# Optimization experiments

Measured on AMD Instinct MI355X. Metric: run time of the kernel, lower is better.

Reference implementation:

```python
import jax, jax.numpy as jnp
import numpy as np

N_NODES = 20000
N_EDGES = 160000
IN_DIM = 2048
HID = 512


def setup_inputs() -> dict:
    key = jax.random.key(0)
    ks = jax.random.split(key, 12)
    s1 = 1.0 / np.sqrt(IN_DIM)
    s2 = 1.0 / np.sqrt(HID)
    return {
        "x": jax.random.normal(ks[0], (N_NODES, IN_DIM), dtype=jnp.float32),
        "edge_index": jax.random.randint(ks[1], (2, N_EDGES), 0, N_NODES, dtype=jnp.int64),
        "W1": jax.random.uniform(ks[2], (IN_DIM, HID), jnp.float32, -s1, s1),
        "b1": jax.random.uniform(ks[3], (HID,), jnp.float32, -s1, s1),
        "W2": jax.random.uniform(ks[4], (HID, HID), jnp.float32, -s2, s2),
        "b2": jax.random.uniform(ks[5], (HID,), jnp.float32, -s2, s2),
        "Wg": jax.random.uniform(ks[6], (HID, HID), jnp.float32, -s2, s2),
        "bg": jax.random.uniform(ks[7], (HID,), jnp.float32, -s2, s2),
        "Wa": jax.random.uniform(ks[8], (HID, 1), jnp.float32, -s2, s2),
        "ba": jax.random.uniform(ks[9], (1,), jnp.float32, -s2, s2),
    }


def reference(x, edge_index, W1, b1, W2, b2, Wg, bg, Wa, ba):
    # GINConv (eps=0): h = MLP((1+eps)*x + sum_{j in N(i)} x_j)
    src, dst = edge_index[0], edge_index[1]
    agg = jax.ops.segment_sum(x[src], dst, num_segments=x.shape[0])  # [N, IN_DIM]
    h = x + agg
    h = jnp.maximum(h @ W1 + b1, 0.0) @ W2 + b2  # [N, HID]
    # Gated attention pooling scores
    A = jnp.tanh(h @ Wg + bg)                    # [N, HID]
    alpha = (A @ Wa + ba)[:, 0]                  # [N]
    att_scores = jax.nn.softmax(alpha, axis=0)   # softmax over all nodes
    return (h, att_scores)
```

## Files before the change

kernel.cpp:

```cpp
#include <hip/hip_runtime.h>

typedef __attribute__((ext_vector_type(8))) __bf16 bf16x8;
typedef __attribute__((ext_vector_type(4))) __bf16 bf16x4;
typedef __attribute__((ext_vector_type(4))) float f32x4;
typedef __attribute__((ext_vector_type(8))) unsigned short u16x8;

__device__ __forceinline__ bf16x8 cvt8(float4 a, float4 b) {
    bf16x8 o;
    o[0] = (__bf16)a.x; o[1] = (__bf16)a.y; o[2] = (__bf16)a.z; o[3] = (__bf16)a.w;
    o[4] = (__bf16)b.x; o[5] = (__bf16)b.y; o[6] = (__bf16)b.z; o[7] = (__bf16)b.w;
    return o;
}
__device__ __forceinline__ bf16x4 cvt4(f32x4 v) {
    bf16x4 o;
    o[0] = (__bf16)v[0]; o[1] = (__bf16)v[1]; o[2] = (__bf16)v[2]; o[3] = (__bf16)v[3];
    return o;
}

__device__ __forceinline__ unsigned swz(int row, int s) {
    return (unsigned)((row * 64 + s * 16) ^ ((row & 8) << 2));
}

__global__ __launch_bounds__(256) void convw_pre_kernel(const float* __restrict__ W,
                                                        char* __restrict__ out, int K) {
    int t = blockIdx.x * 256 + threadIdx.x;
    if (t >= K * 512) return;
    int k = t >> 9, n = t & 511;
    int cb = n >> 8, r = n & 255, tt = k >> 5, s = (k & 31) >> 3, e = k & 7;
    size_t off = ((size_t)cb * (K >> 5) + tt) * 16384 + swz(r, s) + e * 2;
    *(__bf16*)(out + off) = (__bf16)W[t];
}

__global__ __launch_bounds__(256) void count_kernel(const int* __restrict__ dst,
                                                    int* __restrict__ counts, int E) {
    int e = blockIdx.x * 256 + threadIdx.x;
    if (e < E) atomicAdd(&counts[dst[e]], 1);
}

__global__ __launch_bounds__(1024) void scan_kernel(const int* __restrict__ counts,
                                                    int* __restrict__ offs, int N) {
    __shared__ int wsum[16], wpre[16];
    const int CH = 20;
    int tid = threadIdx.x, lane = tid & 63, wv = tid >> 6;
    int base = tid * CH;
    int s = 0;
    for (int i = 0; i < CH; i++) { int idx = base + i; s += (idx < N) ? counts[idx] : 0; }
    int run = s;
#pragma unroll
    for (int o = 1; o < 64; o <<= 1) { int v = __shfl_up(run, o, 64); if (lane >= o) run += v; }
    if (lane == 63) wsum[wv] = run;
    __syncthreads();
    if (tid == 0) { int acc = 0; for (int w = 0; w < 16; w++) { wpre[w] = acc; acc += wsum[w]; } }
    __syncthreads();
    int pre = wpre[wv] + (run - s);
    for (int i = 0; i < CH; i++) {
        int idx = base + i;
        if (idx <= N) offs[idx] = pre;
        pre += (idx < N) ? counts[idx] : 0;
    }
}

__global__ __launch_bounds__(256) void bucket_kernel(const int* __restrict__ src,
                                                     const int* __restrict__ dst,
                                                     const int* __restrict__ offs,
                                                     int* __restrict__ cursor,
                                                     int* __restrict__ eids, int E) {
    int e = blockIdx.x * 256 + threadIdx.x;
    if (e >= E) return;
    int d = dst[e];
    int pos = atomicAdd(&cursor[d], 1);
    eids[offs[d] + pos] = src[e];
}

__global__ __launch_bounds__(256) void gather_h1_kernel(const float* __restrict__ y,
                                                        const int* __restrict__ offs,
                                                        const int* __restrict__ eids,
                                                        const float* __restrict__ b1,
                                                        __bf16* __restrict__ h1b,
                                                        int N) {
    int node = blockIdx.x * 2 + (threadIdx.x >> 7);
    if (node >= N) return;
    int c = (threadIdx.x & 127) << 2;
    float4 s = *(const float4*)(y + (size_t)node * 512 + c);
    int beg = offs[node], end = offs[node + 1];
    for (int k = beg; k < end; k++) {
        int sn = eids[k];
        const float4 v = *(const float4*)(y + (size_t)sn * 512 + c);
        s.x += v.x; s.y += v.y; s.z += v.z; s.w += v.w;
    }
    const float4 b = *(const float4*)(b1 + c);
    f32x4 r;
    r[0] = fmaxf(s.x + b.x, 0.f);
    r[1] = fmaxf(s.y + b.y, 0.f);
    r[2] = fmaxf(s.z + b.z, 0.f);
    r[3] = fmaxf(s.w + b.w, 0.f);
    *(bf16x4*)(h1b + (size_t)node * 512 + c) = cvt4(r);
}

__global__ __launch_bounds__(256) void gemm1_kernel(const float* __restrict__ X,
                                                    const char* __restrict__ Bpre,
                                                    float* __restrict__ Y, int M) {
    constexpr int KDIM = 2048, NT2 = KDIM / 64;
    __shared__ char smem[16384];
    const int tid = threadIdx.x, lane = tid & 63, wv = tid >> 6;
    const int fr = lane & 15, sec = lane >> 4, hi4 = (lane >> 4) * 4;
    const long row0 = (long)blockIdx.x * 64;
    const char* Bp = Bpre + (size_t)blockIdx.y * 64 * 16384;

    f32x4 acc[4][4];
#pragma unroll
    for (int m = 0; m < 4; m++)
#pragma unroll
        for (int n = 0; n < 4; n++)
#pragma unroll
            for (int r = 0; r < 4; r++) acc[m][n][r] = 0.f;

    const int ar_ = tid >> 2, ks = tid & 3;
    const unsigned awz = swz(ar_, ks);
    long arow = row0 + ar_; if (arow > (long)M - 1) arow = M - 1;
    const float* Ap = X + arow * KDIM;

#define ASEC(b) (smem + (b) * 8192)
#define LOAD_A(d0, d1, d2, d3, t) do {                       \
        const float* p_ = Ap + (t) * 64 + ks * 8;            \
        d0 = *(const float4*)(p_);                           \
        d1 = *(const float4*)(p_ + 4);                       \
        d2 = *(const float4*)(p_ + 32);                      \
        d3 = *(const float4*)(p_ + 36);                      \
    } while (0)
#define LOAD_WF(dst, g) do {                                              \
        const char* bt_ = Bp + (size_t)(g) * 16384;                       \
        _Pragma("unroll") for (int m_ = 0; m_ < 4; m_++)                  \
            dst[m_] = *(const bf16x8*)(bt_ + swz(wv * 64 + m_ * 16 + fr, sec)); \
    } while (0)

    float4 aP0, aP1, aP2, aP3, aN0, aN1, aN2, aN3;
    bf16x8 wfC[4], wfN[4];

    LOAD_A(aP0, aP1, aP2, aP3, 0);
    *(bf16x8*)(ASEC(0) + awz) = cvt8(aP0, aP1);
    *(bf16x8*)(ASEC(0) + 4096 + awz) = cvt8(aP2, aP3);
    LOAD_A(aP0, aP1, aP2, aP3, 1);
    LOAD_A(aN0, aN1, aN2, aN3, 2);
    LOAD_WF(wfC, 0);
    asm volatile("s_waitcnt lgkmcnt(0)" ::: "memory");
    __builtin_amdgcn_s_barrier();

    int cur = 0;
    for (int tt = 0; tt < NT2; tt++) {
#pragma unroll
        for (int h = 0; h < 2; h++) {
            const int g = tt * 2 + h;
            if (g + 1 < NT2 * 2) LOAD_WF(wfN, g + 1);
            bf16x8 xf[4];
#pragma unroll
            for (int n = 0; n < 4; n++)
                xf[n] = *(const bf16x8*)(ASEC(cur) + h * 4096 + swz(n * 16 + fr, sec));
#pragma unroll
            for (int m = 0; m < 4; m++)
#pragma unroll
                for (int n = 0; n < 4; n++)
                    acc[m][n] = __builtin_amdgcn_mfma_f32_16x16x32_bf16(wfC[m], xf[n], acc[m][n], 0, 0, 0);
#pragma unroll
            for (int m = 0; m < 4; m++) wfC[m] = wfN[m];
        }
        if (tt + 1 < NT2) {
            const int nxt = cur ^ 1;
            *(bf16x8*)(ASEC(nxt) + awz) = cvt8(aP0, aP1);
            *(bf16x8*)(ASEC(nxt) + 4096 + awz) = cvt8(aP2, aP3);
            aP0 = aN0; aP1 = aN1; aP2 = aN2; aP3 = aN3;
            if (tt + 3 < NT2) LOAD_A(aN0, aN1, aN2, aN3, tt + 3);
            asm volatile("s_waitcnt lgkmcnt(0)" ::: "memory");
            __builtin_amdgcn_s_barrier();
            cur = nxt;
        }
    }
#undef ASEC
#undef LOAD_A
#undef LOAD_WF

#pragma unroll
    for (int n = 0; n < 4; n++) {
        long node = row0 + n * 16 + fr;
        if (node < M) {
#pragma unroll
            for (int m = 0; m < 4; m++)
                *(f32x4*)(Y + node * 512 + blockIdx.y * 256 + wv * 64 + m * 16 + hi4) = acc[m][n];
        }
    }
}

__global__ __launch_bounds__(512) void mlp23_kernel(const __bf16* __restrict__ H1,
                                                    const char* __restrict__ W2p,
                                                    const float* __restrict__ b2,
                                                    const char* __restrict__ Wgp,
                                                    const float* __restrict__ bg,
                                                    const float* __restrict__ Wa,
                                                    float* __restrict__ Hout,
                                                    float* __restrict__ alpha) {
    constexpr int NT2 = 8;
    __shared__ char smem[41216];
    char* Hs = smem + 8192;
    float* aS = (float*)(smem + 40960);
    const int tid = threadIdx.x, lane = tid & 63, wv = tid >> 6;
    const int fr = lane & 15, sec = lane >> 4, hi4 = (lane >> 4) * 4;
    const long row0 = (long)blockIdx.x * 32;
    const int cbv = wv >> 2, rbase = (wv & 3) * 64;

    if (tid < 32) aS[tid] = 0.f;

    const int srow = tid >> 3, sh = (tid & 7) >> 2, ss = tid & 3;
    const unsigned awz = (unsigned)(sh * 2048) + swz(srow, ss);
    const __bf16* ApH = H1 + (row0 + srow) * 512 + sh * 32 + ss * 8;

#define ASEC(b) (smem + (b) * 4096)
#define LOAD_WF(dst, img, g) do {                                         \
        const char* bt_ = (img) + ((size_t)cbv * 16 + (g)) * 16384;       \
        _Pragma("unroll") for (int m_ = 0; m_ < 4; m_++)                  \
            dst[m_] = *(const bf16x8*)(bt_ + swz(rbase + m_ * 16 + fr, sec)); \
    } while (0)

    f32x4 acc[4][2];
#pragma unroll
    for (int m = 0; m < 4; m++)
#pragma unroll
        for (int n = 0; n < 2; n++)
#pragma unroll
            for (int r = 0; r < 4; r++) acc[m][n][r] = 0.f;

    bf16x8 wfC[4], wfN[4];
    if (tid < 256) {
        u16x8 v = *(const u16x8*)(ApH);
        *(u16x8*)(ASEC(0) + awz) = v;
    }
    LOAD_WF(wfC, W2p, 0);
    asm volatile("s_waitcnt lgkmcnt(0)" ::: "memory");
    __builtin_amdgcn_s_barrier();

    int cur = 0;
    for (int tt = 0; tt < NT2; tt++) {
        u16x8 av;
        const bool more = (tt + 1 < NT2);
        if (more && tid < 256) av = *(const u16x8*)(ApH + (tt + 1) * 64);
#pragma unroll
        for (int h = 0; h < 2; h++) {
            const int g = tt * 2 + h;
            if (g + 1 < 16) LOAD_WF(wfN, W2p, g + 1);
            bf16x8 xf[2];
#pragma unroll
            for (int n = 0; n < 2; n++)
                xf[n] = *(const bf16x8*)(ASEC(cur) + h * 2048 + swz(n * 16 + fr, sec));
#pragma unroll
            for (int m = 0; m < 4; m++)
#pragma unroll
                for (int n = 0; n < 2; n++)
                    acc[m][n] = __builtin_amdgcn_mfma_f32_16x16x32_bf16(wfC[m], xf[n], acc[m][n], 0, 0, 0);
#pragma unroll
            for (int m = 0; m < 4; m++) wfC[m] = wfN[m];
        }
        if (more) {
            const int nxt = cur ^ 1;
            if (tid < 256) *(u16x8*)(ASEC(nxt) + awz) = av;
            asm volatile("s_waitcnt lgkmcnt(0)" ::: "memory");
            __builtin_amdgcn_s_barrier();
            cur = nxt;
        }
    }

#pragma unroll
    for (int n = 0; n < 2; n++) {
        int node = n * 16 + fr;
        long gnode = row0 + node;
#pragma unroll
        for (int m = 0; m < 4; m++) {
            int hc = wv * 64 + m * 16 + hi4;
            f32x4 bv = *(const f32x4*)(b2 + hc);
            f32x4 v = acc[m][n] + bv;
            *(f32x4*)(Hout + gnode * 512 + hc) = v;
            int tt = hc >> 5, sk = (hc & 31) >> 3, e = hc & 7;
            *(bf16x4*)(Hs + tt * 2048 + swz(node, sk) + e * 2) = cvt4(v);
        }
    }
    asm volatile("s_waitcnt lgkmcnt(0)" ::: "memory");
    __builtin_amdgcn_s_barrier();

    f32x4 acc2[4][2];
#pragma unroll
    for (int m = 0; m < 4; m++)
#pragma unroll
        for (int n = 0; n < 2; n++)
#pragma unroll
            for (int r = 0; r < 4; r++) acc2[m][n][r] = 0.f;

    LOAD_WF(wfC, Wgp, 0);
    for (int g = 0; g < 16; g++) {
        if (g + 1 < 16) LOAD_WF(wfN, Wgp, g + 1);
        bf16x8 xf[2];
#pragma unroll
        for (int n = 0; n < 2; n++)
            xf[n] = *(const bf16x8*)(Hs + g * 2048 + swz(n * 16 + fr, sec));
#pragma unroll
        for (int m = 0; m < 4; m++)
#pragma unroll
            for (int n = 0; n < 2; n++)
                acc2[m][n] = __builtin_amdgcn_mfma_f32_16x16x32_bf16(wfC[m], xf[n], acc2[m][n], 0, 0, 0);
#pragma unroll
        for (int m = 0; m < 4; m++) wfC[m] = wfN[m];
    }
#undef ASEC
#undef LOAD_WF

#pragma unroll
    for (int n = 0; n < 2; n++) {
        float s = 0.f;
#pragma unroll
        for (int m = 0; m < 4; m++) {
            int gc = wv * 64 + m * 16 + hi4;
            f32x4 bgv = *(const f32x4*)(bg + gc);
            f32x4 wav = *(const f32x4*)(Wa + gc);
#pragma unroll
            for (int r = 0; r < 4; r++)
                s += tanhf(acc2[m][n][r] + bgv[r]) * wav[r];
        }
        s += __shfl_xor(s, 16, 64);
        s += __shfl_xor(s, 32, 64);
        if (sec == 0) atomicAdd(&aS[n * 16 + fr], s);
    }
    __syncthreads();
    if (tid < 32) alpha[row0 + tid] = aS[tid];
}

__global__ __launch_bounds__(1024) void softmax_kernel(const float* __restrict__ alpha,
                                                       float* __restrict__ att, int N) {
    __shared__ float red[16];
    __shared__ float bc[2];
    int tid = threadIdx.x, lane = tid & 63, wv = tid >> 6;
    float m = -3.4e38f;
    for (int i = tid; i < N; i += 1024) m = fmaxf(m, alpha[i]);
#pragma unroll
    for (int o = 32; o > 0; o >>= 1) m = fmaxf(m, __shfl_xor(m, o, 64));
    if (lane == 0) red[wv] = m;
    __syncthreads();
    if (tid == 0) {
        float mm = red[0];
        for (int i = 1; i < 16; i++) mm = fmaxf(mm, red[i]);
        bc[0] = mm;
    }
    __syncthreads();
    float Mx = bc[0];
    float s = 0.f;
    for (int i = tid; i < N; i += 1024) s += expf(alpha[i] - Mx);
#pragma unroll
    for (int o = 32; o > 0; o >>= 1) s += __shfl_xor(s, o, 64);
    if (lane == 0) red[wv] = s;
    __syncthreads();
    if (tid == 0) {
        float ss = 0.f;
        for (int i = 0; i < 16; i++) ss += red[i];
        bc[1] = ss;
    }
    __syncthreads();
    float inv = 1.f / bc[1];
    for (int i = tid; i < N; i += 1024) att[i] = expf(alpha[i] - Mx) * inv;
}

extern "C" void kernel_launch(void* const* d_in, const int* in_sizes, int n_in,
                              void* d_out, int out_size, void* d_ws, size_t ws_size,
                              hipStream_t stream) {
    const float* x  = (const float*)d_in[0];
    const int*   ei = (const int*)d_in[1];
    const float* W1 = (const float*)d_in[2];
    const float* b1 = (const float*)d_in[3];
    const float* W2 = (const float*)d_in[4];
    const float* b2 = (const float*)d_in[5];
    const float* Wg = (const float*)d_in[6];
    const float* bg = (const float*)d_in[7];
    const float* Wa = (const float*)d_in[8];

    const int M = 20000, IN = 2048, H = 512, E = 160000;

    char* ws = (char*)d_ws;
    float* y      = (float*)ws;
    char*  W1p    = ws + 40960000;
    char*  W2p    = ws + 43057152;
    char*  Wgp    = ws + 43581440;
    __bf16* h1b   = (__bf16*)(ws + 44105728);
    float* alpha  = (float*)(ws + 64585728);
    int*   counts = (int*)(ws + 64665728);
    int*   offs   = (int*)(ws + 64745728);
    int*   cursor = (int*)(ws + 64825732);
    int*   eids   = (int*)(ws + 64905732);

    float* hout = (float*)d_out;
    float* att  = hout + (size_t)M * H;

    convw_pre_kernel<<<4096, 256, 0, stream>>>(W1, W1p, IN);
    convw_pre_kernel<<<1024, 256, 0, stream>>>(W2, W2p, H);
    convw_pre_kernel<<<1024, 256, 0, stream>>>(Wg, Wgp, H);

    hipMemsetAsync(counts, 0, M * 4, stream);
    count_kernel<<<(E + 255) / 256, 256, 0, stream>>>(ei + E, counts, E);
    scan_kernel<<<1, 1024, 0, stream>>>(counts, offs, M);
    hipMemsetAsync(cursor, 0, M * 4, stream);
    bucket_kernel<<<(E + 255) / 256, 256, 0, stream>>>(ei, ei + E, offs, cursor, eids, E);

    gemm1_kernel<<<dim3(313, 2), 256, 0, stream>>>(x, W1p, y, M);

    gather_h1_kernel<<<10000, 256, 0, stream>>>(y, offs, eids, b1, h1b, M);

    mlp23_kernel<<<625, 512, 0, stream>>>(h1b, W2p, b2, Wgp, bg, Wa, hout, alpha);

    softmax_kernel<<<1, 1024, 0, stream>>>(alpha, att, M);
}
```

Before: 333.1 us.

## Store intermediate Y in bf16 and shrink gemm1 row tile to 32

The first GEMM now writes its output in bf16 instead of fp32, which halves both the write traffic and the traffic of the neighbor gather that reads it back. The gather kernel moves to 8-element bf16 vectors with four nodes per block. gemm1 uses 32-row tiles and twice as many blocks, and drops the register double-buffering of weight fragments and of the A prefetch, here and in mlp23. This risks exposed load latency in the GEMMs and adds bf16 rounding before the aggregation sum.

```diff
diff --git a/kernel.cpp b/kernel.cpp
--- a/kernel.cpp
+++ b/kernel.cpp
@@ -72,120 +72,102 @@
     eids[offs[d] + pos] = src[e];
 }
 
-__global__ __launch_bounds__(256) void gather_h1_kernel(const float* __restrict__ y,
+__global__ __launch_bounds__(256) void gather_h1_kernel(const __bf16* __restrict__ y,
                                                         const int* __restrict__ offs,
                                                         const int* __restrict__ eids,
                                                         const float* __restrict__ b1,
-                                                        __bf16* __restrict__ h1b,
-                                                        int N) {
-    int node = blockIdx.x * 2 + (threadIdx.x >> 7);
-    if (node >= N) return;
-    int c = (threadIdx.x & 127) << 2;
-    float4 s = *(const float4*)(y + (size_t)node * 512 + c);
-    int beg = offs[node], end = offs[node + 1];
+                                                        __bf16* __restrict__ h1b) {
+    const int node = blockIdx.x * 4 + (threadIdx.x >> 6);
+    const int c = (threadIdx.x & 63) * 8;
+    float s[8];
+    bf16x8 v = *(const bf16x8*)(y + (size_t)node * 512 + c);
+#pragma unroll
+    for (int j = 0; j < 8; j++) s[j] = (float)v[j];
+    const int beg = offs[node], end = offs[node + 1];
     for (int k = beg; k < end; k++) {
         int sn = eids[k];
-        const float4 v = *(const float4*)(y + (size_t)sn * 512 + c);
-        s.x += v.x; s.y += v.y; s.z += v.z; s.w += v.w;
-    }
-    const float4 b = *(const float4*)(b1 + c);
-    f32x4 r;
-    r[0] = fmaxf(s.x + b.x, 0.f);
-    r[1] = fmaxf(s.y + b.y, 0.f);
-    r[2] = fmaxf(s.z + b.z, 0.f);
-    r[3] = fmaxf(s.w + b.w, 0.f);
-    *(bf16x4*)(h1b + (size_t)node * 512 + c) = cvt4(r);
+        bf16x8 u = *(const bf16x8*)(y + (size_t)sn * 512 + c);
+#pragma unroll
+        for (int j = 0; j < 8; j++) s[j] += (float)u[j];
+    }
+    bf16x8 o;
+#pragma unroll
+    for (int j = 0; j < 8; j++) o[j] = (__bf16)fmaxf(s[j] + b1[c + j], 0.f);
+    *(bf16x8*)(h1b + (size_t)node * 512 + c) = o;
 }
 
 __global__ __launch_bounds__(256) void gemm1_kernel(const float* __restrict__ X,
                                                     const char* __restrict__ Bpre,
-                                                    float* __restrict__ Y, int M) {
+                                                    __bf16* __restrict__ Y) {
     constexpr int KDIM = 2048, NT2 = KDIM / 64;
-    __shared__ char smem[16384];
+    __shared__ char smem[8192];
     const int tid = threadIdx.x, lane = tid & 63, wv = tid >> 6;
     const int fr = lane & 15, sec = lane >> 4, hi4 = (lane >> 4) * 4;
-    const long row0 = (long)blockIdx.x * 64;
+    const int row0 = blockIdx.x * 32;
     const char* Bp = Bpre + (size_t)blockIdx.y * 64 * 16384;
 
-    f32x4 acc[4][4];
+    f32x4 acc[4][2];
 #pragma unroll
     for (int m = 0; m < 4; m++)
 #pragma unroll
-        for (int n = 0; n < 4; n++)
+        for (int n = 0; n < 2; n++)
 #pragma unroll
             for (int r = 0; r < 4; r++) acc[m][n][r] = 0.f;
 
-    const int ar_ = tid >> 2, ks = tid & 3;
-    const unsigned awz = swz(ar_, ks);
-    long arow = row0 + ar_; if (arow > (long)M - 1) arow = M - 1;
-    const float* Ap = X + arow * KDIM;
-
-#define ASEC(b) (smem + (b) * 8192)
-#define LOAD_A(d0, d1, d2, d3, t) do {                       \
-        const float* p_ = Ap + (t) * 64 + ks * 8;            \
-        d0 = *(const float4*)(p_);                           \
-        d1 = *(const float4*)(p_ + 4);                       \
-        d2 = *(const float4*)(p_ + 32);                      \
-        d3 = *(const float4*)(p_ + 36);                      \
-    } while (0)
-#define LOAD_WF(dst, g) do {                                              \
-        const char* bt_ = Bp + (size_t)(g) * 16384;                       \
-        _Pragma("unroll") for (int m_ = 0; m_ < 4; m_++)                  \
-            dst[m_] = *(const bf16x8*)(bt_ + swz(wv * 64 + m_ * 16 + fr, sec)); \
-    } while (0)
-
-    float4 aP0, aP1, aP2, aP3, aN0, aN1, aN2, aN3;
-    bf16x8 wfC[4], wfN[4];
-
-    LOAD_A(aP0, aP1, aP2, aP3, 0);
-    *(bf16x8*)(ASEC(0) + awz) = cvt8(aP0, aP1);
-    *(bf16x8*)(ASEC(0) + 4096 + awz) = cvt8(aP2, aP3);
-    LOAD_A(aP0, aP1, aP2, aP3, 1);
-    LOAD_A(aN0, aN1, aN2, aN3, 2);
-    LOAD_WF(wfC, 0);
+    const int r_ = tid >> 3, h_ = (tid & 7) >> 2, s_ = tid & 3;
+    const unsigned awz = (unsigned)(h_ * 2048) + swz(r_, s_);
+    const float* Ap = X + (size_t)(row0 + r_) * KDIM + h_ * 32 + s_ * 8;
+
+#define ASEC(b) (smem + (b) * 4096)
+
+    {
+        float4 a0 = *(const float4*)(Ap), a1 = *(const float4*)(Ap + 4);
+        *(bf16x8*)(ASEC(0) + awz) = cvt8(a0, a1);
+    }
     asm volatile("s_waitcnt lgkmcnt(0)" ::: "memory");
     __builtin_amdgcn_s_barrier();
 
     int cur = 0;
     for (int tt = 0; tt < NT2; tt++) {
+        const bool more = (tt + 1 < NT2);
+        float4 a0, a1;
+        if (more) {
+            a0 = *(const float4*)(Ap + (tt + 1) * 64);
+            a1 = *(const float4*)(Ap + (tt + 1) * 64 + 4);
+        }
 #pragma unroll
         for (int h = 0; h < 2; h++) {
-            const int g = tt * 2 + h;
-            if (g + 1 < NT2 * 2) LOAD_WF(wfN, g + 1);
-            bf16x8 xf[4];
-#pragma unroll
-            for (int n = 0; n < 4; n++)
-                xf[n] = *(const bf16x8*)(ASEC(cur) + h * 4096 + swz(n * 16 + fr, sec));
+            const char* bt = Bp + (size_t)(tt * 2 + h) * 16384;
+            bf16x8 wf[4], xf[2];
 #pragma unroll
             for (int m = 0; m < 4; m++)
-#pragma unroll
-                for (int n = 0; n < 4; n++)
-                    acc[m][n] = __builtin_amdgcn_mfma_f32_16x16x32_bf16(wfC[m], xf[n], acc[m][n], 0, 0, 0);
-#pragma unroll
-            for (int m = 0; m < 4; m++) wfC[m] = wfN[m];
-        }
-        if (tt + 1 < NT2) {
+                wf[m] = *(const bf16x8*)(bt + swz(wv * 64 + m * 16 + fr, sec));
+#pragma unroll
+            for (int n = 0; n < 2; n++)
+                xf[n] = *(const bf16x8*)(ASEC(cur) + h * 2048 + swz(n * 16 + fr, sec));
+#pragma unroll
+            for (int m = 0; m < 4; m++)
+#pragma unroll
+                for (int n = 0; n < 2; n++)
+                    acc[m][n] = __builtin_amdgcn_mfma_f32_16x16x32_bf16(wf[m], xf[n], acc[m][n], 0, 0, 0);
+        }
+        if (more) {
             const int nxt = cur ^ 1;
-            *(bf16x8*)(ASEC(nxt) + awz) = cvt8(aP0, aP1);
-            *(bf16x8*)(ASEC(nxt) + 4096 + awz) = cvt8(aP2, aP3);
-            aP0 = aN0; aP1 = aN1; aP2 = aN2; aP3 = aN3;
-            if (tt + 3 < NT2) LOAD_A(aN0, aN1, aN2, aN3, tt + 3);
+            *(bf16x8*)(ASEC(nxt) + awz) = cvt8(a0, a1);
             asm volatile("s_waitcnt lgkmcnt(0)" ::: "memory");
             __builtin_amdgcn_s_barrier();
             cur = nxt;
         }
     }
 #undef ASEC
-#undef LOAD_A
-#undef LOAD_WF
-
-#pragma unroll
-    for (int n = 0; n < 4; n++) {
-        long node = row0 + n * 16 + fr;
-        if (node < M) {
-#pragma unroll
-            for (int m = 0; m < 4; m++)
-                *(f32x4*)(Y + node * 512 + blockIdx.y * 256 + wv * 64 + m * 16 + hi4) = acc[m][n];
+
+#pragma unroll
+    for (int n = 0; n < 2; n++) {
+        int node = row0 + n * 16 + fr;
+#pragma unroll
+        for (int m = 0; m < 4; m++) {
+            int col = blockIdx.y * 256 + wv * 64 + m * 16 + hi4;
+            *(bf16x4*)(Y + (size_t)node * 512 + col) = cvt4(acc[m][n]);
         }
     }
 }
@@ -214,11 +196,6 @@
     const __bf16* ApH = H1 + (row0 + srow) * 512 + sh * 32 + ss * 8;
 
 #define ASEC(b) (smem + (b) * 4096)
-#define LOAD_WF(dst, img, g) do {                                         \
-        const char* bt_ = (img) + ((size_t)cbv * 16 + (g)) * 16384;       \
-        _Pragma("unroll") for (int m_ = 0; m_ < 4; m_++)                  \
-            dst[m_] = *(const bf16x8*)(bt_ + swz(rbase + m_ * 16 + fr, sec)); \
-    } while (0)
 
     f32x4 acc[4][2];
 #pragma unroll
@@ -228,12 +205,10 @@
 #pragma unroll
             for (int r = 0; r < 4; r++) acc[m][n][r] = 0.f;
 
-    bf16x8 wfC[4], wfN[4];
     if (tid < 256) {
         u16x8 v = *(const u16x8*)(ApH);
         *(u16x8*)(ASEC(0) + awz) = v;
     }
-    LOAD_WF(wfC, W2p, 0);
     asm volatile("s_waitcnt lgkmcnt(0)" ::: "memory");
     __builtin_amdgcn_s_barrier();
 
@@ -244,9 +219,11 @@
         if (more && tid < 256) av = *(const u16x8*)(ApH + (tt + 1) * 64);
 #pragma unroll
         for (int h = 0; h < 2; h++) {
-            const int g = tt * 2 + h;
-            if (g + 1 < 16) LOAD_WF(wfN, W2p, g + 1);
-            bf16x8 xf[2];
+            const char* bt = W2p + ((size_t)cbv * 16 + tt * 2 + h) * 16384;
+            bf16x8 wf[4], xf[2];
+#pragma unroll
+            for (int m = 0; m < 4; m++)
+                wf[m] = *(const bf16x8*)(bt + swz(rbase + m * 16 + fr, sec));
 #pragma unroll
             for (int n = 0; n < 2; n++)
                 xf[n] = *(const bf16x8*)(ASEC(cur) + h * 2048 + swz(n * 16 + fr, sec));
@@ -254,9 +231,7 @@
             for (int m = 0; m < 4; m++)
 #pragma unroll
                 for (int n = 0; n < 2; n++)
-                    acc[m][n] = __builtin_amdgcn_mfma_f32_16x16x32_bf16(wfC[m], xf[n], acc[m][n], 0, 0, 0);
-#pragma unroll
-            for (int m = 0; m < 4; m++) wfC[m] = wfN[m];
+                    acc[m][n] = __builtin_amdgcn_mfma_f32_16x16x32_bf16(wf[m], xf[n], acc[m][n], 0, 0, 0);
         }
         if (more) {
             const int nxt = cur ^ 1;
@@ -292,10 +267,12 @@
 #pragma unroll
             for (int r = 0; r < 4; r++) acc2[m][n][r] = 0.f;
 
-    LOAD_WF(wfC, Wgp, 0);
     for (int g = 0; g < 16; g++) {
-        if (g + 1 < 16) LOAD_WF(wfN, Wgp, g + 1);
-        bf16x8 xf[2];
+        const char* bt = Wgp + ((size_t)cbv * 16 + g) * 16384;
+        bf16x8 wf[4], xf[2];
+#pragma unroll
+        for (int m = 0; m < 4; m++)
+            wf[m] = *(const bf16x8*)(bt + swz(rbase + m * 16 + fr, sec));
 #pragma unroll
         for (int n = 0; n < 2; n++)
             xf[n] = *(const bf16x8*)(Hs + g * 2048 + swz(n * 16 + fr, sec));
@@ -303,12 +280,9 @@
         for (int m = 0; m < 4; m++)
 #pragma unroll
             for (int n = 0; n < 2; n++)
-                acc2[m][n] = __builtin_amdgcn_mfma_f32_16x16x32_bf16(wfC[m], xf[n], acc2[m][n], 0, 0, 0);
-#pragma unroll
-        for (int m = 0; m < 4; m++) wfC[m] = wfN[m];
+                acc2[m][n] = __builtin_amdgcn_mfma_f32_16x16x32_bf16(wf[m], xf[n], acc2[m][n], 0, 0, 0);
     }
 #undef ASEC
-#undef LOAD_WF
 
 #pragma unroll
     for (int n = 0; n < 2; n++) {
@@ -380,16 +354,16 @@
     const int M = 20000, IN = 2048, H = 512, E = 160000;
 
     char* ws = (char*)d_ws;
-    float* y      = (float*)ws;
-    char*  W1p    = ws + 40960000;
-    char*  W2p    = ws + 43057152;
-    char*  Wgp    = ws + 43581440;
-    __bf16* h1b   = (__bf16*)(ws + 44105728);
-    float* alpha  = (float*)(ws + 64585728);
-    int*   counts = (int*)(ws + 64665728);
-    int*   offs   = (int*)(ws + 64745728);
-    int*   cursor = (int*)(ws + 64825732);
-    int*   eids   = (int*)(ws + 64905732);
+    __bf16* ybf   = (__bf16*)ws;
+    char*  W1p    = ws + 20480000;
+    char*  W2p    = ws + 22577152;
+    char*  Wgp    = ws + 23101440;
+    __bf16* h1b   = (__bf16*)(ws + 23625728);
+    float* alpha  = (float*)(ws + 44105728);
+    int*   counts = (int*)(ws + 44185728);
+    int*   offs   = (int*)(ws + 44265728);
+    int*   cursor = (int*)(ws + 44345732);
+    int*   eids   = (int*)(ws + 44425732);
 
     float* hout = (float*)d_out;
     float* att  = hout + (size_t)M * H;
@@ -404,9 +378,9 @@
     hipMemsetAsync(cursor, 0, M * 4, stream);
     bucket_kernel<<<(E + 255) / 256, 256, 0, stream>>>(ei, ei + E, offs, cursor, eids, E);
 
-    gemm1_kernel<<<dim3(313, 2), 256, 0, stream>>>(x, W1p, y, M);
-
-    gather_h1_kernel<<<10000, 256, 0, stream>>>(y, offs, eids, b1, h1b, M);
+    gemm1_kernel<<<dim3(625, 2), 256, 0, stream>>>(x, W1p, ybf);
+
+    gather_h1_kernel<<<5000, 256, 0, stream>>>(ybf, offs, eids, b1, h1b);
 
     mlp23_kernel<<<625, 512, 0, stream>>>(h1b, W2p, b2, Wgp, bg, Wa, hout, alpha);
 
```

After: 318.2 us. 1.05x faster.
